# Kernel tuning notes

Measured on AMD Instinct MI355X. Metric: run time of the kernel, lower is better.

The kernel has to match this reference:

```python
import jax, jax.numpy as jnp
import numpy as np

BN_EPS = 1e-5


def _fps(xyz, n_centers):
    """Furthest point sampling. xyz: (B,N,3) -> idx (B,n_centers) int32.
    Deterministic start at index 0 (torch version uses randint start)."""
    B, N, _ = xyz.shape
    batch_ar = jnp.arange(B)

    def step(carry, _):
        distances, farthest = carry  # (B,N), (B,)
        center = xyz[batch_ar, farthest]  # (B,3)
        d = jnp.sum((xyz - center[:, None, :]) ** 2, axis=-1)  # (B,N)
        distances = jnp.minimum(distances, d)
        new_far = jnp.argmax(distances, axis=-1)
        return (distances, new_far), farthest

    init = (jnp.full((B, N), jnp.inf, dtype=xyz.dtype),
            jnp.zeros((B,), dtype=jnp.int32))
    _, idxs = jax.lax.scan(step, init, None, length=n_centers)  # (n_centers, B)
    return idxs.T  # (B, n_centers)


def _knn_group(xyz, centers, k):
    """xyz:(B,N,3), centers:(B,M,3) -> patches (B,M,k,3) center-relative."""
    # (B,M,N) squared distances
    dists = jnp.sum((centers[:, :, None, :] - xyz[:, None, :, :]) ** 2, axis=-1)
    _, idx = jax.lax.top_k(-dists, k)  # (B,M,k) smallest distances
    # gather neighbor coords: (B,M,k,3)
    patches = jnp.take_along_axis(xyz[:, None, :, :], idx[..., None], axis=2)
    return patches - centers[:, :, None, :]


def _bn_eval(x, gamma, beta):
    # BatchNorm1d in eval mode: running_mean=0, running_var=1
    return x * (gamma / jnp.sqrt(1.0 + BN_EPS)) + beta


def _mini_pointnet(patches, W1, b1, g1, bt1, W2, b2, g2, bt2, W3, b3, g3, bt3):
    B, M, k, C = patches.shape
    x = patches.reshape(B * M * k, C)
    x = jax.nn.relu(_bn_eval(x @ W1 + b1, g1, bt1))
    x = jax.nn.relu(_bn_eval(x @ W2 + b2, g2, bt2))
    x = jax.nn.relu(_bn_eval(x @ W3 + b3, g3, bt3))
    x = x.reshape(B * M, k, -1).max(axis=1)
    return x.reshape(B, M, -1)


def setup_inputs() -> dict:
    key = jax.random.key(0)
    ks = jax.random.split(key, 8)
    B, N = 16, 16384
    embed = 256

    def lin(kk, fan_in, fan_out):
        bound = 1.0 / np.sqrt(fan_in)
        k1, k2 = jax.random.split(kk)
        W = jax.random.uniform(k1, (fan_in, fan_out), jnp.float32, -bound, bound)
        b = jax.random.uniform(k2, (fan_out,), jnp.float32, -bound, bound)
        return W, b

    W1, b1 = lin(ks[1], 3, 64)
    W2, b2 = lin(ks[2], 64, 128)
    W3, b3 = lin(ks[3], 128, embed)
    return {
        "xyz": jax.random.normal(ks[0], (B, N, 3), jnp.float32),
        "W1": W1, "b1": b1, "g1": jnp.ones((64,)), "bt1": jnp.zeros((64,)),
        "W2": W2, "b2": b2, "g2": jnp.ones((128,)), "bt2": jnp.zeros((128,)),
        "W3": W3, "b3": b3, "g3": jnp.ones((embed,)), "bt3": jnp.zeros((embed,)),
        "n_centers": 256,
        "k": 32,
    }


def reference(xyz, W1, b1, g1, bt1, W2, b2, g2, bt2, W3, b3, g3, bt3,
              n_centers, k):
    center_idx = _fps(xyz, n_centers)  # (B, M)
    centers = jnp.take_along_axis(xyz, center_idx[..., None], axis=1)  # (B,M,3)
    patches = _knn_group(xyz, centers, k)  # (B,M,k,3)
    tokens = _mini_pointnet(patches, W1, b1, g1, bt1, W2, b2, g2, bt2,
                            W3, b3, g3, bt3)
    return tokens, centers
```

## Files before the change

kernel.cpp:

```cpp
#include <hip/hip_runtime.h>

constexpr int B   = 16;
constexpr int N   = 16384;
constexpr int M   = 256;
constexpr int K   = 32;
constexpr int EMB = 256;

__device__ __forceinline__ float sqdist(float px, float py, float pz,
                                        float cx, float cy, float cz) {
  float dx = __fsub_rn(px, cx);
  float dy = __fsub_rn(py, cy);
  float dz = __fsub_rn(pz, cz);
  return __fadd_rn(__fadd_rn(__fmul_rn(dx, dx), __fmul_rn(dy, dy)),
                   __fmul_rn(dz, dz));
}

constexpr int FT = 1024;
constexpr int FW = FT / 64;

__global__ __launch_bounds__(FT) void fps_kernel(
    const float* __restrict__ xyz, float* __restrict__ centers) {
  const int b = blockIdx.x;
  const int tid = threadIdx.x;
  const float* base = xyz + (size_t)b * N * 3;
  const float4* b4 = (const float4*)base;

  __shared__ float4 s_co[6 * FT];
  __shared__ float4 s_dA[3 * FT];
  __shared__ float s_pv[2][FW];
  __shared__ int s_pn[2][FW];

  const int f0 = tid * 12;
#pragma unroll
  for (int c = 0; c < 6; ++c) s_co[c * FT + tid] = b4[f0 + c];
  const float inf = __builtin_inff();
#pragma unroll
  for (int c = 0; c < 3; ++c) s_dA[c * FT + tid] = make_float4(inf, inf, inf, inf);
  float ds12 = inf, ds13 = inf, ds14 = inf, ds15 = inf;

  float cx = base[0], cy = base[1], cz = base[2];
  __syncthreads();

  for (int it = 0; it < M; ++it) {
    if (tid == 0) {
      float* co = centers + ((size_t)b * M + it) * 3;
      co[0] = cx; co[1] = cy; co[2] = cz;
    }
    const int p = it & 1;

    float bv = -1.0f;
    int bj = 0;

#define FPS_UPD(D, J, X, Y, Z) {                           \
    float dx = __fsub_rn((X), cx);                         \
    float dy = __fsub_rn((Y), cy);                         \
    float dz = __fsub_rn((Z), cz);                         \
    float dd = __fadd_rn(__fadd_rn(__fmul_rn(dx, dx),      \
                                   __fmul_rn(dy, dy)),     \
                         __fmul_rn(dz, dz));               \
    float nd = fminf(D, dd);                               \
    D = nd;                                                \
    bool g = nd > bv;                                      \
    bv = g ? nd : bv;                                      \
    bj = g ? (J) : bj; }

#define FPS_G4(qa, qb, qc, D0, D1, D2, D3, JB)             \
    FPS_UPD(D0, (JB) + 0, qa.x, qa.y, qa.z)                \
    FPS_UPD(D1, (JB) + 1, qa.w, qb.x, qb.y)                \
    FPS_UPD(D2, (JB) + 2, qb.z, qb.w, qc.x)                \
    FPS_UPD(D3, (JB) + 3, qc.y, qc.z, qc.w)

    float4 g0 = b4[f0 + 6], g1 = b4[f0 + 7], g2 = b4[f0 + 8];

    {
      float4 qa = s_co[0 * FT + tid];
      float4 qb = s_co[1 * FT + tid];
      float4 qc = s_co[2 * FT + tid];
      float4 dq = s_dA[0 * FT + tid];
      FPS_G4(qa, qb, qc, dq.x, dq.y, dq.z, dq.w, 0)
      s_dA[0 * FT + tid] = dq;
    }
    float4 g3 = b4[f0 + 9], g4 = b4[f0 + 10], g5 = b4[f0 + 11];
    {
      float4 qa = s_co[3 * FT + tid];
      float4 qb = s_co[4 * FT + tid];
      float4 qc = s_co[5 * FT + tid];
      float4 dq = s_dA[1 * FT + tid];
      FPS_G4(qa, qb, qc, dq.x, dq.y, dq.z, dq.w, 4)
      s_dA[1 * FT + tid] = dq;
    }
    {
      float4 dq = s_dA[2 * FT + tid];
      FPS_G4(g0, g1, g2, dq.x, dq.y, dq.z, dq.w, 8)
      s_dA[2 * FT + tid] = dq;
    }
    FPS_G4(g3, g4, g5, ds12, ds13, ds14, ds15, 12)
#undef FPS_G4
#undef FPS_UPD

    int bn = (tid << 4) + bj;

#pragma unroll
    for (int mm = 32; mm >= 1; mm >>= 1) {
      float ov = __shfl_xor(bv, mm, 64);
      int on = __shfl_xor(bn, mm, 64);
      if (ov > bv || (ov == bv && on < bn)) { bv = ov; bn = on; }
    }
    if ((tid & 63) == 0) { s_pv[p][tid >> 6] = bv; s_pn[p][tid >> 6] = bn; }
    __syncthreads();

    float v = s_pv[p][0];
    int n = s_pn[p][0];
#pragma unroll
    for (int w = 1; w < FW; ++w) {
      float ov = s_pv[p][w];
      int on = s_pn[p][w];
      if (ov > v || (ov == v && on < n)) { v = ov; n = on; }
    }
    cx = base[(size_t)n * 3 + 0];
    cy = base[(size_t)n * 3 + 1];
    cz = base[(size_t)n * 3 + 2];
  }
}

constexpr int KT = 256;
constexpr int CAP = 512;
constexpr int NBUCKET = 1024;

__global__ __launch_bounds__(KT) void knn_kernel(
    const float* __restrict__ xyz, const float* __restrict__ centers,
    float* __restrict__ patches) {
  const int blk = blockIdx.x;
  const int b = blk >> 8;
  const int tid = threadIdx.x;
  const float* base = xyz + (size_t)b * N * 3;

  __shared__ int hist[NBUCKET];
  __shared__ unsigned cb[CAP];
  __shared__ int ci[CAP];
  __shared__ int s_nin, s_ncand, s_tb;
  __shared__ int s_wsum[KT / 64];
  __shared__ float s_cc[3];

  if (tid == 0) {
    const float* c = centers + (size_t)blk * 3;
    s_cc[0] = c[0]; s_cc[1] = c[1]; s_cc[2] = c[2];
    s_nin = 0; s_ncand = 0;
  }
  for (int i = tid; i < NBUCKET; i += KT) hist[i] = 0;
  __syncthreads();

  const float cx = s_cc[0], cy = s_cc[1], cz = s_cc[2];

  for (int n = tid; n < N; n += KT) {
    float d = sqdist(base[n * 3], base[n * 3 + 1], base[n * 3 + 2], cx, cy, cz);
    atomicAdd(&hist[__float_as_uint(d) >> 21], 1);
  }
  __syncthreads();

  int h0[4];
  int loc = 0;
#pragma unroll
  for (int i = 0; i < 4; ++i) { h0[i] = hist[tid * 4 + i]; loc += h0[i]; }
  int lane = tid & 63, wid = tid >> 6;
  int scan = loc;
  for (int off = 1; off < 64; off <<= 1) {
    int o = __shfl_up(scan, off, 64);
    if (lane >= off) scan += o;
  }
  if (lane == 63) s_wsum[wid] = scan;
  __syncthreads();
  int woff = 0;
  for (int w = 0; w < wid; ++w) woff += s_wsum[w];
  int c0 = woff + scan - loc;
#pragma unroll
  for (int i = 0; i < 4; ++i) {
    int c1 = c0 + h0[i];
    if (c0 < K && c1 >= K) s_tb = tid * 4 + i;
    c0 = c1;
  }
  __syncthreads();
  const int tb = s_tb;
  const unsigned lo = (unsigned)tb << 21;
  const unsigned hi = (unsigned)(tb + 1) << 21;

  for (int n = tid; n < N; n += KT) {
    float x = base[n * 3], y = base[n * 3 + 1], z = base[n * 3 + 2];
    float d = sqdist(x, y, z, cx, cy, cz);
    unsigned bits = __float_as_uint(d);
    if (bits < lo) {
      int pos = atomicAdd(&s_nin, 1);
      float* p = patches + ((size_t)blk * K + pos) * 3;
      p[0] = __fsub_rn(x, cx); p[1] = __fsub_rn(y, cy); p[2] = __fsub_rn(z, cz);
    } else if (bits < hi) {
      int q = atomicAdd(&s_ncand, 1);
      if (q < CAP) { cb[q] = bits; ci[q] = n; }
    }
  }
  __syncthreads();

  const int nin = s_nin;
  const int ncand = min(s_ncand, CAP);
  const int nsel = K - nin;
  for (int j = tid; j < ncand; j += KT) {
    unsigned bj = cb[j];
    int ij = ci[j];
    int rank = 0;
    for (int i2 = 0; i2 < ncand; ++i2) {
      unsigned bv = cb[i2];
      int iv = ci[i2];
      rank += (bv < bj || (bv == bj && iv < ij)) ? 1 : 0;
    }
    if (rank < nsel) {
      float x = base[ij * 3], y = base[ij * 3 + 1], z = base[ij * 3 + 2];
      float* p = patches + ((size_t)blk * K + nin + rank) * 3;
      p[0] = __fsub_rn(x, cx); p[1] = __fsub_rn(y, cy); p[2] = __fsub_rn(z, cz);
    }
  }
}

constexpr int MT = 128;

__global__ __launch_bounds__(MT) void mlp_kernel(
    const float* __restrict__ patches,
    const float* __restrict__ W1, const float* __restrict__ b1,
    const float* __restrict__ g1, const float* __restrict__ bt1,
    const float* __restrict__ W2, const float* __restrict__ b2,
    const float* __restrict__ g2, const float* __restrict__ bt2,
    const float* __restrict__ W3, const float* __restrict__ b3,
    const float* __restrict__ g3, const float* __restrict__ bt3,
    float* __restrict__ tokens) {
  const int pm = blockIdx.x;
  const int tid = threadIdx.x;
  __shared__ float xs[3][K];
  __shared__ float h1s[64 * K];
  __shared__ float h2s[128 * K];
  __shared__ float pms[2][EMB];

  const float* patch = patches + (size_t)pm * (K * 3);
  if (tid < 96) xs[tid % 3][tid / 3] = patch[tid];
  __syncthreads();

  const int cg = tid & 63;
  const int half = tid >> 6;
  const int pt0 = half * 16;
  const float rs = 1.0f / sqrtf(1.0f + 1e-5f);

  {
    const int c = cg;
    const float w0 = W1[c], w1 = W1[64 + c], w2 = W1[128 + c];
    const float bb = b1[c];
    const float sc = g1[c] * rs, be = bt1[c];
    float o[16];
#pragma unroll
    for (int p = 0; p < 16; ++p) {
      int pt = pt0 + p;
      float a = xs[0][pt] * w0 + xs[1][pt] * w1 + xs[2][pt] * w2 + bb;
      o[p] = fmaxf(a * sc + be, 0.0f);
    }
    const int so = (c & 7) << 2;
#pragma unroll
    for (int p4 = 0; p4 < 16; p4 += 4) {
      *(float4*)&h1s[c * K + ((pt0 + p4) ^ so)] =
          make_float4(o[p4], o[p4 + 1], o[p4 + 2], o[p4 + 3]);
    }
  }
  __syncthreads();

  {
    const int c = cg * 2;
    float acc0[16], acc1[16];
    const float bb0 = b2[c], bb1 = b2[c + 1];
#pragma unroll
    for (int p = 0; p < 16; ++p) { acc0[p] = bb0; acc1[p] = bb1; }
    for (int k = 0; k < 64; ++k) {
      const float2 w = *(const float2*)(W2 + k * 128 + c);
      const int so = (k & 7) << 2;
      float4 x0 = *(const float4*)&h1s[k * K + ((pt0 + 0) ^ so)];
      float4 x1 = *(const float4*)&h1s[k * K + ((pt0 + 4) ^ so)];
      float4 x2 = *(const float4*)&h1s[k * K + ((pt0 + 8) ^ so)];
      float4 x3 = *(const float4*)&h1s[k * K + ((pt0 + 12) ^ so)];
      float xv[16] = {x0.x, x0.y, x0.z, x0.w, x1.x, x1.y, x1.z, x1.w,
                      x2.x, x2.y, x2.z, x2.w, x3.x, x3.y, x3.z, x3.w};
#pragma unroll
      for (int p = 0; p < 16; ++p) {
        acc0[p] += xv[p] * w.x;
        acc1[p] += xv[p] * w.y;
      }
    }
    const float sc0 = g2[c] * rs, be0 = bt2[c];
    const float sc1 = g2[c + 1] * rs, be1 = bt2[c + 1];
    float o0[16], o1[16];
#pragma unroll
    for (int p = 0; p < 16; ++p) {
      o0[p] = fmaxf(acc0[p] * sc0 + be0, 0.0f);
      o1[p] = fmaxf(acc1[p] * sc1 + be1, 0.0f);
    }
    const int soa = (c & 7) << 2, sob = ((c + 1) & 7) << 2;
#pragma unroll
    for (int p4 = 0; p4 < 16; p4 += 4) {
      *(float4*)&h2s[c * K + ((pt0 + p4) ^ soa)] =
          make_float4(o0[p4], o0[p4 + 1], o0[p4 + 2], o0[p4 + 3]);
      *(float4*)&h2s[(c + 1) * K + ((pt0 + p4) ^ sob)] =
          make_float4(o1[p4], o1[p4 + 1], o1[p4 + 2], o1[p4 + 3]);
    }
  }
  __syncthreads();

  {
    const int c = cg * 4;
    float acc[4][16];
#pragma unroll
    for (int i = 0; i < 4; ++i) {
      const float bb = b3[c + i];
#pragma unroll
      for (int p = 0; p < 16; ++p) acc[i][p] = bb;
    }
    for (int k = 0; k < 128; ++k) {
      const float4 w = *(const float4*)(W3 + (size_t)k * 256 + c);
      const int so = (k & 7) << 2;
      float4 x0 = *(const float4*)&h2s[k * K + ((pt0 + 0) ^ so)];
      float4 x1 = *(const float4*)&h2s[k * K + ((pt0 + 4) ^ so)];
      float4 x2 = *(const float4*)&h2s[k * K + ((pt0 + 8) ^ so)];
      float4 x3 = *(const float4*)&h2s[k * K + ((pt0 + 12) ^ so)];
      float xv[16] = {x0.x, x0.y, x0.z, x0.w, x1.x, x1.y, x1.z, x1.w,
                      x2.x, x2.y, x2.z, x2.w, x3.x, x3.y, x3.z, x3.w};
#pragma unroll
      for (int p = 0; p < 16; ++p) {
        acc[0][p] += xv[p] * w.x;
        acc[1][p] += xv[p] * w.y;
        acc[2][p] += xv[p] * w.z;
        acc[3][p] += xv[p] * w.w;
      }
    }
#pragma unroll
    for (int i = 0; i < 4; ++i) {
      const float sc = g3[c + i] * rs, be = bt3[c + i];
      float mx = 0.0f;
#pragma unroll
      for (int p = 0; p < 16; ++p)
        mx = fmaxf(mx, fmaxf(acc[i][p] * sc + be, 0.0f));
      pms[half][c + i] = mx;
    }
  }
  __syncthreads();

  {
    const int c2 = tid * 2;
    float* to = tokens + (size_t)pm * EMB;
    to[c2] = fmaxf(pms[0][c2], pms[1][c2]);
    to[c2 + 1] = fmaxf(pms[0][c2 + 1], pms[1][c2 + 1]);
  }
}

extern "C" void kernel_launch(void* const* d_in, const int* in_sizes, int n_in,
                              void* d_out, int out_size, void* d_ws,
                              size_t ws_size, hipStream_t stream) {
  const float* xyz = (const float*)d_in[0];
  const float* W1 = (const float*)d_in[1];
  const float* b1 = (const float*)d_in[2];
  const float* g1 = (const float*)d_in[3];
  const float* bt1 = (const float*)d_in[4];
  const float* W2 = (const float*)d_in[5];
  const float* b2 = (const float*)d_in[6];
  const float* g2 = (const float*)d_in[7];
  const float* bt2 = (const float*)d_in[8];
  const float* W3 = (const float*)d_in[9];
  const float* b3 = (const float*)d_in[10];
  const float* g3 = (const float*)d_in[11];
  const float* bt3 = (const float*)d_in[12];

  float* tokens = (float*)d_out;
  float* centers = tokens + (size_t)B * M * EMB;
  float* patches = (float*)d_ws;

  fps_kernel<<<B, FT, 0, stream>>>(xyz, centers);
  knn_kernel<<<B * M, KT, 0, stream>>>(xyz, centers, patches);
  mlp_kernel<<<B * M, MT, 0, stream>>>(patches, W1, b1, g1, bt1, W2, b2, g2,
                                       bt2, W3, b3, g3, bt3, tokens);
}
```

Baseline: 993.6 us.

## Replace FPS barrier with LDS flag spin-wait and shuffle-based cross-wave reduction

The per-iteration __syncthreads in furthest point sampling is replaced by per-wave flags in shared memory that every wave spins on until all 16 waves have published their partial argmax. The final reduction over 16 wave results now uses 16-lane shuffles instead of a serial loop. Point coordinates are no longer staged in shared memory and are reloaded from global memory each iteration, with all distances kept in LDS. The intent is to cut barrier and serial-reduction latency on the sequential FPS loop. In exchange it relies on LDS ordering and the double-buffered partial slots for correctness, and adds repeated global loads per iteration.

```diff
diff --git a/kernel.cpp b/kernel.cpp
--- a/kernel.cpp
+++ b/kernel.cpp
@@ -22,24 +22,26 @@
     const float* __restrict__ xyz, float* __restrict__ centers) {
   const int b = blockIdx.x;
   const int tid = threadIdx.x;
+  const int lane = tid & 63;
+  const int wid = tid >> 6;
+  const int l15 = lane & 15;
   const float* base = xyz + (size_t)b * N * 3;
   const float4* b4 = (const float4*)base;
 
-  __shared__ float4 s_co[6 * FT];
-  __shared__ float4 s_dA[3 * FT];
+  __shared__ float4 s_d[4][FT];
   __shared__ float s_pv[2][FW];
   __shared__ int s_pn[2][FW];
+  __shared__ int s_flag[FW];
+
+  const float inf = __builtin_inff();
+#pragma unroll
+  for (int c = 0; c < 4; ++c) s_d[c][tid] = make_float4(inf, inf, inf, inf);
+  if (tid < FW) s_flag[tid] = 0;
+
+  float cx = base[0], cy = base[1], cz = base[2];
+  __syncthreads();
 
   const int f0 = tid * 12;
-#pragma unroll
-  for (int c = 0; c < 6; ++c) s_co[c * FT + tid] = b4[f0 + c];
-  const float inf = __builtin_inff();
-#pragma unroll
-  for (int c = 0; c < 3; ++c) s_dA[c * FT + tid] = make_float4(inf, inf, inf, inf);
-  float ds12 = inf, ds13 = inf, ds14 = inf, ds15 = inf;
-
-  float cx = base[0], cy = base[1], cz = base[2];
-  __syncthreads();
 
   for (int it = 0; it < M; ++it) {
     if (tid == 0) {
@@ -64,38 +66,18 @@
     bv = g ? nd : bv;                                      \
     bj = g ? (J) : bj; }
 
-#define FPS_G4(qa, qb, qc, D0, D1, D2, D3, JB)             \
-    FPS_UPD(D0, (JB) + 0, qa.x, qa.y, qa.z)                \
-    FPS_UPD(D1, (JB) + 1, qa.w, qb.x, qb.y)                \
-    FPS_UPD(D2, (JB) + 2, qb.z, qb.w, qc.x)                \
-    FPS_UPD(D3, (JB) + 3, qc.y, qc.z, qc.w)
-
-    float4 g0 = b4[f0 + 6], g1 = b4[f0 + 7], g2 = b4[f0 + 8];
-
-    {
-      float4 qa = s_co[0 * FT + tid];
-      float4 qb = s_co[1 * FT + tid];
-      float4 qc = s_co[2 * FT + tid];
-      float4 dq = s_dA[0 * FT + tid];
-      FPS_G4(qa, qb, qc, dq.x, dq.y, dq.z, dq.w, 0)
-      s_dA[0 * FT + tid] = dq;
-    }
-    float4 g3 = b4[f0 + 9], g4 = b4[f0 + 10], g5 = b4[f0 + 11];
-    {
-      float4 qa = s_co[3 * FT + tid];
-      float4 qb = s_co[4 * FT + tid];
-      float4 qc = s_co[5 * FT + tid];
-      float4 dq = s_dA[1 * FT + tid];
-      FPS_G4(qa, qb, qc, dq.x, dq.y, dq.z, dq.w, 4)
-      s_dA[1 * FT + tid] = dq;
-    }
-    {
-      float4 dq = s_dA[2 * FT + tid];
-      FPS_G4(g0, g1, g2, dq.x, dq.y, dq.z, dq.w, 8)
-      s_dA[2 * FT + tid] = dq;
-    }
-    FPS_G4(g3, g4, g5, ds12, ds13, ds14, ds15, 12)
-#undef FPS_G4
+#pragma unroll
+    for (int c = 0; c < 4; ++c) {
+      float4 qa = b4[f0 + c * 3 + 0];
+      float4 qb = b4[f0 + c * 3 + 1];
+      float4 qc = b4[f0 + c * 3 + 2];
+      float4 dq = s_d[c][tid];
+      FPS_UPD(dq.x, c * 4 + 0, qa.x, qa.y, qa.z)
+      FPS_UPD(dq.y, c * 4 + 1, qa.w, qb.x, qb.y)
+      FPS_UPD(dq.z, c * 4 + 2, qb.z, qb.w, qc.x)
+      FPS_UPD(dq.w, c * 4 + 3, qc.y, qc.z, qc.w)
+      s_d[c][tid] = dq;
+    }
 #undef FPS_UPD
 
     int bn = (tid << 4) + bj;
@@ -106,15 +88,26 @@
       int on = __shfl_xor(bn, mm, 64);
       if (ov > bv || (ov == bv && on < bn)) { bv = ov; bn = on; }
     }
-    if ((tid & 63) == 0) { s_pv[p][tid >> 6] = bv; s_pn[p][tid >> 6] = bn; }
-    __syncthreads();
-
-    float v = s_pv[p][0];
-    int n = s_pn[p][0];
-#pragma unroll
-    for (int w = 1; w < FW; ++w) {
-      float ov = s_pv[p][w];
-      int on = s_pn[p][w];
+
+    if (lane == 0) {
+      s_pv[p][wid] = bv;
+      s_pn[p][wid] = bn;
+      asm volatile("s_waitcnt lgkmcnt(0)" ::: "memory");
+      s_flag[wid] = it + 1;
+    }
+
+    {
+      volatile int* vf = s_flag;
+      while (!__all(vf[l15] >= it + 1)) {}
+    }
+    asm volatile("" ::: "memory");
+
+    float v = s_pv[p][l15];
+    int n = s_pn[p][l15];
+#pragma unroll
+    for (int mm = 1; mm <= 8; mm <<= 1) {
+      float ov = __shfl_xor(v, mm, 16);
+      int on = __shfl_xor(n, mm, 16);
       if (ov > v || (ov == v && on < n)) { v = ov; n = on; }
     }
     cx = base[(size_t)n * 3 + 0];
```

Result: faster. 835.7 us (-15.9%).
